# Performance work log

Measured on AMD Instinct MI355X. Metric: run time of the kernel, lower is better.

Reference implementation:

```python
import jax, jax.numpy as jnp
import numpy as np

N_NODES = 20000


def _gcn_norm(edge_index, n):
    src, dst = edge_index[0], edge_index[1]
    # degree of A + I (self-loops), all edge weights 1
    deg = jax.ops.segment_sum(jnp.ones(src.shape[0], jnp.float32), dst, num_segments=n) + 1.0
    dinv = jax.lax.rsqrt(deg)
    norm = dinv[src] * dinv[dst]          # [E]
    self_norm = dinv * dinv               # [N] self-loop coefficient = 1/deg
    return src, dst, norm, self_norm


def _gcn_layer(x, W, b, src, dst, norm, self_norm):
    # x: [B, N, Fin]; W: [Fin, Fout]
    h = jnp.einsum('bnf,fo->bno', x, W)   # transform first (PyG GCNConv order)
    msg = h[:, src, :] * norm[None, :, None]                      # [B, E, Fout]
    agg = jax.vmap(lambda m: jax.ops.segment_sum(m, dst, num_segments=x.shape[1]))(msg)
    agg = agg + h * self_norm[None, :, None]                      # self-loop term
    return agg + b


def setup_inputs() -> dict:
    key = jax.random.key(0)
    ks = jax.random.split(key, 8)
    B, N, Fin, H, O, E = 2, N_NODES, 256, 256, 64, 320000
    s = lambda f: 1.0 / np.sqrt(f)
    return {
        'x': jax.random.normal(ks[0], (B, N, Fin), jnp.float32),
        'W1': jax.random.normal(ks[1], (Fin, H), jnp.float32) * s(Fin),
        'b1': jnp.zeros((H,), jnp.float32),
        'W2': jax.random.normal(ks[2], (H, H), jnp.float32) * s(H),
        'b2': jnp.zeros((H,), jnp.float32),
        'Wfc': jax.random.normal(ks[3], (H, O), jnp.float32) * s(H),
        'bfc': jnp.zeros((O,), jnp.float32),
        'edge_index': jax.random.randint(ks[4], (2, E), 0, N, jnp.int64),
    }


def reference(x, W1, b1, W2, b2, Wfc, bfc, edge_index):
    src, dst, norm, self_norm = _gcn_norm(edge_index, x.shape[1])
    h = jax.nn.relu(_gcn_layer(x, W1, b1, src, dst, norm, self_norm))
    h = jax.nn.relu(_gcn_layer(h, W2, b2, src, dst, norm, self_norm))
    pooled = jnp.mean(h, axis=1)          # mean over nodes -> [B, H]
    return pooled @ Wfc + bfc             # [B, O]
```

## Files before the change

kernel.cpp:

```cpp
#include <hip/hip_runtime.h>

#define NNODES 20000
#define BATCH  2
#define FEAT   256
#define OOUT   64
#define PBLK2  400
#define MROWS  40000
#define NPB    20096
#define H8ROWS 40192
#define NCHUNK 20

typedef short  bhalf8 __attribute__((ext_vector_type(8)));
typedef float  floatx4 __attribute__((ext_vector_type(4)));
typedef float  floatx2 __attribute__((ext_vector_type(2)));

__device__ __forceinline__ float bf2f(unsigned short u) {
  return __uint_as_float(((unsigned int)u) << 16);
}
__device__ __forceinline__ unsigned short f2bf(float f) {
  unsigned int u = __float_as_uint(f);
  return (unsigned short)((u + 0x7fffu + ((u >> 16) & 1u)) >> 16);
}
__device__ __forceinline__ unsigned int pack4_fp8(float a, float b, float c, float d) {
  int p = __builtin_amdgcn_cvt_pk_fp8_f32(a, b, 0, false);
  p = __builtin_amdgcn_cvt_pk_fp8_f32(c, d, p, true);
  return (unsigned int)p;
}

__global__ __launch_bounds__(256) void prep_kernel(const float* __restrict__ W1,
                                                   const float* __restrict__ W2,
                                                   unsigned short* __restrict__ w1hi,
                                                   unsigned short* __restrict__ w1lo,
                                                   unsigned short* __restrict__ w2hi,
                                                   unsigned short* __restrict__ w2lo,
                                                   const int* __restrict__ raw, int E,
                                                   int* __restrict__ flag,
                                                   int* __restrict__ cnt,
                                                   int* __restrict__ fill,
                                                   int* __restrict__ chunkOff) {
  int bid = blockIdx.x, tid = threadIdx.x;
  int idx = bid * 256 + tid;
  int which = idx >> 16, loc = idx & 65535;
  const float* W = which ? W2 : W1;
  unsigned short* Whi = which ? w2hi : w1hi;
  unsigned short* Wlo = which ? w2lo : w1lo;
  int k = loc >> 8, n = loc & 255;
  float w = W[loc];
  unsigned short hi = f2bf(w);
  unsigned short lo = f2bf(w - bf2f(hi));
  int g = n >> 4, ln = n & 15;
  int ks = k >> 5, ch = (k >> 3) & 3, j = k & 7;
  int addr = ((ks * 16 + g) * 64 + ch * 16 + ln) * 8 + j;
  Whi[addr] = hi;
  Wlo[addr] = lo;
  if (idx < NNODES) { cnt[idx] = 0; fill[idx] = 0; }
  if (idx < NCHUNK) chunkOff[idx] = 0;
  if (bid == 511) {
    __shared__ int any;
    if (tid == 0) any = 0;
    __syncthreads();
    int nchk = E < 2048 ? E : 2048;
    for (int i = tid; i < nchk; i += 256)
      if (raw[2 * i + 1] != 0) any = 1;
    __syncthreads();
    if (tid == 0) *flag = any;
  }
}

__global__ void count_kernel(const int* __restrict__ raw, const int* __restrict__ flag,
                             int* __restrict__ cnt, int E) {
  int e = blockIdx.x * blockDim.x + threadIdx.x;
  if (e >= E) return;
  int d = (*flag) ? raw[E + e] : raw[2 * (E + e)];
  atomicAdd(&cnt[d], 1);
}

__global__ __launch_bounds__(256) void scan_a_kernel(const int* __restrict__ cnt,
                                                     int* __restrict__ row_start,
                                                     float* __restrict__ dinv,
                                                     int* __restrict__ chunkOff) {
  int c = blockIdx.x, tid = threadIdx.x;
  int base = c * 1024 + tid * 4;
  int v[4]; int tsum = 0;
#pragma unroll
  for (int j = 0; j < 4; ++j) {
    v[j] = (base + j < NNODES) ? cnt[base + j] : 0;
    tsum += v[j];
  }
  int lane = tid & 63, wv = tid >> 6;
  int x = tsum;
#pragma unroll
  for (int off = 1; off < 64; off <<= 1) {
    int t = __shfl_up(x, off);
    if (lane >= off) x += t;
  }
  __shared__ int wsum[4];
  if (lane == 63) wsum[wv] = x;
  __syncthreads();
  int woff = 0;
  for (int w = 0; w < wv; ++w) woff += wsum[w];
  int run = woff + x - tsum;
#pragma unroll
  for (int j = 0; j < 4; ++j) {
    if (base + j <= NNODES) row_start[base + j] = run;
    if (base + j < NNODES) dinv[base + j] = 1.0f / sqrtf((float)(v[j] + 1));
    run += v[j];
  }
  if (tid == 0) {
    int T = wsum[0] + wsum[1] + wsum[2] + wsum[3];
    for (int c2 = c + 1; c2 < NCHUNK; ++c2) atomicAdd(&chunkOff[c2], T);
  }
}

__global__ void scatter_kernel(const int* __restrict__ raw, const int* __restrict__ flag,
                               const int* __restrict__ row_start, const int* __restrict__ chunkOff,
                               int* __restrict__ fill, const float* __restrict__ dinv,
                               int* __restrict__ csr_src, float* __restrict__ csr_norm, int E) {
  int e = blockIdx.x * blockDim.x + threadIdx.x;
  if (e >= E) return;
  int s, d;
  if (*flag) { s = raw[e];     d = raw[E + e]; }
  else       { s = raw[2 * e]; d = raw[2 * (E + e)]; }
  int p = row_start[d] + chunkOff[d >> 10] + atomicAdd(&fill[d], 1);
  csr_src[p] = s;
  csr_norm[p] = dinv[s] * dinv[d];
}

template <int AFP32>
__global__ __launch_bounds__(256) void gemm_mfma(const void* __restrict__ Av,
                                                 const unsigned short* __restrict__ Whi,
                                                 const unsigned short* __restrict__ Wlo,
                                                 unsigned int* __restrict__ C) {
  int bid = blockIdx.x;
  int tile = (bid >> 4) * 8 + (bid & 7);
  int half = (bid >> 3) & 1;
  if (tile >= 314) return;
  __shared__ unsigned short lds[2][8192];
  int b = tile >= 157 ? 1 : 0;
  int nbase = (tile - b * 157) * 128;
  int tid = threadIdx.x, lane = tid & 63, wv = tid >> 6;
  int kc = (lane >> 4) * 8;

  const float* Af          = (const float*)Av;
  const unsigned short* Ab = (const unsigned short*)Av;

  int nn[2], mr[2];
#pragma unroll
  for (int t = 0; t < 2; ++t) {
    int nl = nbase + wv * 32 + t * 16 + (lane & 15);
    nn[t] = nl;
    int ncl = nl > NNODES - 1 ? NNODES - 1 : nl;
    mr[t] = b * NNODES + ncl;
  }

  floatx4 acc[2][8];
#pragma unroll
  for (int t = 0; t < 2; ++t)
#pragma unroll
    for (int g = 0; g < 8; ++g) acc[t][g] = (floatx4)(0.0f);

  bhalf8 st[4];
  auto stage_load = [&](int ks) {
#pragma unroll
    for (int i2 = 0; i2 < 4; ++i2) {
      int u = i2 * 256 + tid;
      int hl = u >> 9, g = (u >> 6) & 7, l = u & 63;
      const unsigned short* Wp = hl ? Wlo : Whi;
      st[i2] = *(const bhalf8*)&Wp[((size_t)(ks * 16 + half * 8 + g) * 64 + l) * 8];
    }
  };
  auto stage_write = [&](int buf) {
#pragma unroll
    for (int i2 = 0; i2 < 4; ++i2) {
      int u = i2 * 256 + tid;
      *(bhalf8*)&lds[buf][(size_t)u * 8] = st[i2];
    }
  };
  auto load_a = [&](int ks, bhalf8 (&a)[2]) {
#pragma unroll
    for (int t = 0; t < 2; ++t) {
      if (AFP32) {
        const float* p = &Af[(size_t)mr[t] * FEAT + ks * 32 + kc];
        float4 u = *(const float4*)p;
        float4 v = *(const float4*)(p + 4);
        a[t][0] = (short)f2bf(u.x); a[t][1] = (short)f2bf(u.y);
        a[t][2] = (short)f2bf(u.z); a[t][3] = (short)f2bf(u.w);
        a[t][4] = (short)f2bf(v.x); a[t][5] = (short)f2bf(v.y);
        a[t][6] = (short)f2bf(v.z); a[t][7] = (short)f2bf(v.w);
      } else {
        a[t] = *(const bhalf8*)&Ab[(size_t)mr[t] * FEAT + ks * 32 + kc];
      }
    }
  };
  auto step = [&](int buf, bhalf8 (&a)[2]) {
#pragma unroll
    for (int g = 0; g < 8; ++g) {
      bhalf8 bh = *(const bhalf8*)&lds[buf][((size_t)g * 64 + lane) * 8];
      bhalf8 bl = *(const bhalf8*)&lds[buf][((size_t)(512 + g * 64) + lane) * 8];
#pragma unroll
      for (int t = 0; t < 2; ++t)
        acc[t][g] = __builtin_amdgcn_mfma_f32_16x16x32_bf16(bh, a[t], acc[t][g], 0, 0, 0);
#pragma unroll
      for (int t = 0; t < 2; ++t)
        acc[t][g] = __builtin_amdgcn_mfma_f32_16x16x32_bf16(bl, a[t], acc[t][g], 0, 0, 0);
    }
  };

  stage_load(0);
  stage_write(0);
  __syncthreads();
  bhalf8 aC[2];
  load_a(0, aC);
  int cur = 0;
#pragma unroll
  for (int ks = 0; ks < 8; ++ks) {
    bhalf8 aN[2];
    if (ks < 7) {
      stage_load(ks + 1);
      load_a(ks + 1, aN);
    }
    step(cur, aC);
    if (ks < 7) {
      stage_write(cur ^ 1);
      __syncthreads();
      aC[0] = aN[0]; aC[1] = aN[1];
    }
    cur ^= 1;
  }

  int nc = (lane >> 4) * 4;
#pragma unroll
  for (int t = 0; t < 2; ++t) {
    size_t r = (size_t)nn[t] * 2 + b;
#pragma unroll
    for (int g = 0; g < 8; ++g) {
      int col = (half * 8 + g) * 16 + nc;
      C[r * 64 + (col >> 2)] =
          pack4_fp8(acc[t][g][0], acc[t][g][1], acc[t][g][2], acc[t][g][3]);
    }
  }
}

__global__ __launch_bounds__(128) void agg_kernel(const uint4* __restrict__ h8,
                                                  const int* __restrict__ row_start,
                                                  const int* __restrict__ chunkOff,
                                                  const int* __restrict__ csr_src,
                                                  const float* __restrict__ csr_norm,
                                                  const float* __restrict__ dinv,
                                                  const float* __restrict__ bias,
                                                  unsigned short* __restrict__ out) {
  int n = blockIdx.x;
  int tid = threadIdx.x;
  int wave = tid >> 6, lane = tid & 63;
  int q = (wave << 1) | (lane >> 5);
  int cl = lane & 31;

  float a[16];
#pragma unroll
  for (int j = 0; j < 16; ++j) a[j] = 0.0f;

  auto dec_fma = [&](uint4 m, float w) {
    unsigned int mm[4] = {m.x, m.y, m.z, m.w};
#pragma unroll
    for (int j = 0; j < 4; ++j) {
      floatx2 lo = __builtin_amdgcn_cvt_pk_f32_fp8((int)mm[j], false);
      floatx2 hi = __builtin_amdgcn_cvt_pk_f32_fp8((int)mm[j], true);
      a[j * 4 + 0] = fmaf(w, lo[0], a[j * 4 + 0]);
      a[j * 4 + 1] = fmaf(w, lo[1], a[j * 4 + 1]);
      a[j * 4 + 2] = fmaf(w, hi[0], a[j * 4 + 2]);
      a[j * 4 + 3] = fmaf(w, hi[1], a[j * 4 + 3]);
    }
  };

  float di = dinv[n];
  if (q == 0) dec_fma(h8[(size_t)n * 32 + cl], di * di);

  int s0 = row_start[n] + chunkOff[n >> 10];
  int s1 = row_start[n + 1] + chunkOff[(n + 1) >> 10];
  int i = s0 + q;
  for (; i + 4 < s1; i += 8) {
    int sa = csr_src[i], sb = csr_src[i + 4];
    float wa = csr_norm[i], wb = csr_norm[i + 4];
    uint4 ma = h8[(size_t)sa * 32 + cl];
    uint4 mb = h8[(size_t)sb * 32 + cl];
    dec_fma(ma, wa);
    dec_fma(mb, wb);
  }
  if (i < s1) dec_fma(h8[(size_t)csr_src[i] * 32 + cl], csr_norm[i]);

#pragma unroll
  for (int j = 0; j < 16; ++j) a[j] += __shfl_xor(a[j], 32);

  __shared__ float red[32][17];
  if (wave == 1 && lane < 32) {
#pragma unroll
    for (int j = 0; j < 16; ++j) red[lane][j] = a[j];
  }
  __syncthreads();
  if (wave == 0 && lane < 32) {
    int b = cl >> 4;
    int c = (cl & 15) * 16;
#pragma unroll
    for (int j = 0; j < 16; ++j) a[j] += red[lane][j];
    unsigned short o[16];
#pragma unroll
    for (int j = 0; j < 16; ++j)
      o[j] = f2bf(fmaxf(a[j] + bias[c + j], 0.0f));
    unsigned short* dst = &out[((size_t)b * NNODES + n) * FEAT + c];
    *(uint4*)dst = *(uint4*)&o[0];
    *(uint4*)(dst + 8) = *(uint4*)&o[8];
  }
}

__global__ __launch_bounds__(256) void pool_partial(const uint4* __restrict__ h2u,
                                                    float* __restrict__ partials) {
  int blk = blockIdx.x;
  int tid = threadIdx.x;
  int rg = tid >> 5, cl = tid & 31;
  int rend = blk * 100 + 100;
  float acc[8];
#pragma unroll
  for (int j = 0; j < 8; ++j) acc[j] = 0.0f;
  for (int r = blk * 100 + rg; r < rend; r += 8) {
    uint4 m = h2u[(size_t)r * 32 + cl];
    unsigned int mm[4] = {m.x, m.y, m.z, m.w};
#pragma unroll
    for (int j = 0; j < 4; ++j) {
      acc[2 * j + 0] += bf2f((unsigned short)(mm[j] & 0xffffu));
      acc[2 * j + 1] += bf2f((unsigned short)(mm[j] >> 16));
    }
  }
  __shared__ float red[8][256];
#pragma unroll
  for (int j = 0; j < 8; ++j) red[rg][cl * 8 + j] = acc[j];
  __syncthreads();
  float s = red[0][tid] + red[1][tid] + red[2][tid] + red[3][tid]
          + red[4][tid] + red[5][tid] + red[6][tid] + red[7][tid];
  partials[(size_t)blk * 256 + tid] = s;
}

__global__ __launch_bounds__(256) void pool_fc(const float* __restrict__ partials,
                                               const float* __restrict__ Wfc,
                                               const float* __restrict__ bfc,
                                               float* __restrict__ out) {
  __shared__ float pooled[BATCH][FEAT];
  int t = threadIdx.x;
  float s0 = 0.f, s1 = 0.f;
  for (int p = 0; p < PBLK2 / 2; ++p) {
    s0 += partials[(size_t)p * 256 + t];
    s1 += partials[(size_t)(PBLK2 / 2 + p) * 256 + t];
  }
  pooled[0][t] = s0 / (float)NNODES;
  pooled[1][t] = s1 / (float)NNODES;
  __syncthreads();
  if (t < BATCH * OOUT) {
    int b = t >> 6, o = t & 63;
    float acc = bfc[o];
    for (int c2 = 0; c2 < FEAT; ++c2)
      acc = fmaf(pooled[b][c2], Wfc[c2 * OOUT + o], acc);
    out[b * OOUT + o] = acc;
  }
}

extern "C" void kernel_launch(void* const* d_in, const int* in_sizes, int n_in,
                              void* d_out, int out_size, void* d_ws, size_t ws_size,
                              hipStream_t stream) {
  const float* x    = (const float*)d_in[0];
  const float* W1   = (const float*)d_in[1];
  const float* b1   = (const float*)d_in[2];
  const float* W2   = (const float*)d_in[3];
  const float* b2   = (const float*)d_in[4];
  const float* Wfc  = (const float*)d_in[5];
  const float* bfc  = (const float*)d_in[6];
  const int*   eraw = (const int*)d_in[7];
  int E = in_sizes[7] / 2;
  float* out = (float*)d_out;

  char* ws = (char*)d_ws;
  size_t off = 0;
  auto alloc = [&](size_t elems4B) -> void* {
    void* p = ws + off * 4;
    off += (elems4B + 3) & ~(size_t)3;
    return p;
  };
  int*   flag      = (int*)alloc(4);
  int*   cnt       = (int*)alloc(NNODES);
  float* dinv      = (float*)alloc(NNODES);
  int*   row_start = (int*)alloc(NNODES + 1);
  int*   fill      = (int*)alloc(NNODES);
  int*   chunkOff  = (int*)alloc(NCHUNK + 4);
  int*   csr_src   = (int*)alloc(E);
  float* csr_norm  = (float*)alloc(E);
  unsigned short* w1hi = (unsigned short*)alloc(65536 / 2);
  unsigned short* w1lo = (unsigned short*)alloc(65536 / 2);
  unsigned short* w2hi = (unsigned short*)alloc(65536 / 2);
  unsigned short* w2lo = (unsigned short*)alloc(65536 / 2);
  unsigned int*   h8   = (unsigned int*)alloc((size_t)H8ROWS * 64);
  unsigned short* a1   = (unsigned short*)alloc((size_t)MROWS * FEAT / 2);
  float* partials  = (float*)alloc((size_t)PBLK2 * 256);

  int eg = (E + 255) / 256;
  prep_kernel<<<512, 256, 0, stream>>>(W1, W2, w1hi, w1lo, w2hi, w2lo, eraw, E, flag,
                                       cnt, fill, chunkOff);
  count_kernel<<<eg, 256, 0, stream>>>(eraw, flag, cnt, E);
  scan_a_kernel<<<NCHUNK, 256, 0, stream>>>(cnt, row_start, dinv, chunkOff);
  scatter_kernel<<<eg, 256, 0, stream>>>(eraw, flag, row_start, chunkOff, fill, dinv,
                                         csr_src, csr_norm, E);

  gemm_mfma<1><<<640, 256, 0, stream>>>(x, w1hi, w1lo, h8);
  agg_kernel<<<NNODES, 128, 0, stream>>>((const uint4*)h8, row_start, chunkOff,
                                         csr_src, csr_norm, dinv, b1, a1);
  gemm_mfma<0><<<640, 256, 0, stream>>>(a1, w2hi, w2lo, h8);
  agg_kernel<<<NNODES, 128, 0, stream>>>((const uint4*)h8, row_start, chunkOff,
                                         csr_src, csr_norm, dinv, b2, a1);
  pool_partial<<<PBLK2, 256, 0, stream>>>((const uint4*)a1, partials);
  pool_fc<<<1, 256, 0, stream>>>(partials, Wfc, bfc, out);
}
```

Baseline: 176.4 us.

## Split aggregation across batch and feature halves with 16 edge slots per block

The aggregation kernel now launches four blocks per node, one for each (batch, feature-half) pair. Each block covers 8 uint4 columns with 16 edge slots instead of 32 columns with 4 slots, and the partial sums are reduced with extra warp shuffles. This raises parallelism and in-flight gathers per row. In exchange it launches four times as many blocks, and every block re-reads the CSR indices and weights.

```diff
diff --git a/kernel.cpp b/kernel.cpp
--- a/kernel.cpp
+++ b/kernel.cpp
@@ -249,11 +249,15 @@
                                                   const float* __restrict__ dinv,
                                                   const float* __restrict__ bias,
                                                   unsigned short* __restrict__ out) {
-  int n = blockIdx.x;
+  int bid = blockIdx.x;
+  int s = bid / NNODES;
+  int n = bid - s * NNODES;
+  int b = s & 1, h = s >> 1;
   int tid = threadIdx.x;
   int wave = tid >> 6, lane = tid & 63;
-  int q = (wave << 1) | (lane >> 5);
-  int cl = lane & 31;
+  int slot = (wave << 3) | (lane >> 3);
+  int cl = lane & 7;
+  int ubase = b * 16 + h * 8 + cl;
 
   float a[16];
 #pragma unroll
@@ -273,33 +277,30 @@
   };
 
   float di = dinv[n];
-  if (q == 0) dec_fma(h8[(size_t)n * 32 + cl], di * di);
+  if (slot == 0) dec_fma(h8[(size_t)n * 32 + ubase], di * di);
 
   int s0 = row_start[n] + chunkOff[n >> 10];
   int s1 = row_start[n + 1] + chunkOff[(n + 1) >> 10];
-  int i = s0 + q;
-  for (; i + 4 < s1; i += 8) {
-    int sa = csr_src[i], sb = csr_src[i + 4];
-    float wa = csr_norm[i], wb = csr_norm[i + 4];
-    uint4 ma = h8[(size_t)sa * 32 + cl];
-    uint4 mb = h8[(size_t)sb * 32 + cl];
-    dec_fma(ma, wa);
-    dec_fma(mb, wb);
-  }
-  if (i < s1) dec_fma(h8[(size_t)csr_src[i] * 32 + cl], csr_norm[i]);
-
-#pragma unroll
-  for (int j = 0; j < 16; ++j) a[j] += __shfl_xor(a[j], 32);
-
-  __shared__ float red[32][17];
-  if (wave == 1 && lane < 32) {
+  for (int i = s0 + slot; i < s1; i += 16) {
+    int sa = csr_src[i];
+    float wa = csr_norm[i];
+    dec_fma(h8[(size_t)sa * 32 + ubase], wa);
+  }
+
+#pragma unroll
+  for (int j = 0; j < 16; ++j) {
+    a[j] += __shfl_xor(a[j], 8);
+    a[j] += __shfl_xor(a[j], 16);
+    a[j] += __shfl_xor(a[j], 32);
+  }
+  __shared__ float red[8][17];
+  if (wave == 1 && lane < 8) {
 #pragma unroll
     for (int j = 0; j < 16; ++j) red[lane][j] = a[j];
   }
   __syncthreads();
-  if (wave == 0 && lane < 32) {
-    int b = cl >> 4;
-    int c = (cl & 15) * 16;
+  if (wave == 0 && lane < 8) {
+    int c = h * 128 + cl * 16;
 #pragma unroll
     for (int j = 0; j < 16; ++j) a[j] += red[lane][j];
     unsigned short o[16];
@@ -408,11 +409,11 @@
                                          csr_src, csr_norm, E);
 
   gemm_mfma<1><<<640, 256, 0, stream>>>(x, w1hi, w1lo, h8);
-  agg_kernel<<<NNODES, 128, 0, stream>>>((const uint4*)h8, row_start, chunkOff,
-                                         csr_src, csr_norm, dinv, b1, a1);
+  agg_kernel<<<4 * NNODES, 128, 0, stream>>>((const uint4*)h8, row_start, chunkOff,
+                                             csr_src, csr_norm, dinv, b1, a1);
   gemm_mfma<0><<<640, 256, 0, stream>>>(a1, w2hi, w2lo, h8);
-  agg_kernel<<<NNODES, 128, 0, stream>>>((const uint4*)h8, row_start, chunkOff,
-                                         csr_src, csr_norm, dinv, b2, a1);
+  agg_kernel<<<4 * NNODES, 128, 0, stream>>>((const uint4*)h8, row_start, chunkOff,
+                                             csr_src, csr_norm, dinv, b2, a1);
   pool_partial<<<PBLK2, 256, 0, stream>>>((const uint4*)a1, partials);
   pool_fc<<<1, 256, 0, stream>>>(partials, Wfc, bfc, out);
 }
```

Result: slower. 305.3 us (+73.1%).
